# Kernel optimization log

Measured on AMD Instinct MI355X. Metric: run time of the kernel, lower is better.

The kernel has to match this reference:

```python
import jax, jax.numpy as jnp
import numpy as np

GAE_GAMMA = 0.99
GAE_LAMBDA = 0.95
T, N_ENVS = 4096, 2048


def setup_inputs() -> dict:
    key = jax.random.key(0)
    k1, k2, k3, k4 = jax.random.split(key, 4)
    rewards = jax.random.normal(k1, (T, N_ENVS), dtype=jnp.float32)
    values = jax.random.normal(k2, (T, N_ENVS), dtype=jnp.float32)
    next_values = jax.random.normal(k3, (T, N_ENVS), dtype=jnp.float32)
    next_dones = jax.random.randint(k4, (T, N_ENVS), 0, 2).astype(jnp.bool_)
    return {"rewards": rewards, "values": values,
            "next_values": next_values, "next_dones": next_dones}


def reference(rewards, values, next_values, next_dones):
    gamma = jnp.asarray(GAE_GAMMA, rewards.dtype)
    lam = jnp.asarray(GAE_LAMBDA, rewards.dtype)
    not_done = 1.0 - next_dones.astype(rewards.dtype)  # ~next_dones
    # deltas[t] = r[t] + gamma * V(s_{t+1}) * ~done[t] - V(s_t)
    deltas = rewards + gamma * next_values * not_done - values
    gae_discount = gamma * lam

    def step(running_gae, inp):
        delta_t, nd_t = inp
        g = delta_t + gae_discount * nd_t * running_gae
        return g, g

    init = jnp.zeros_like(rewards[0])
    # reverse-time scan over the recurrence
    _, adv = jax.lax.scan(step, init, (deltas, not_done), reverse=True)
    returns = adv + values
    return adv, returns
```

## Files before the change

kernel.cpp:

```cpp
#include <hip/hip_runtime.h>

#define TT    4096
#define NENV  2048
#define N4    (NENV / 4)
#define L     8
#define NCH   (TT / L)
#define TPCH  (NENV / 4)
#define NCGRP (TPCH / 256)
#define NBLK  (NCH * NCGRP)

#define GAMMA 0.99f
#define GL    (0.99f * 0.95f)

#define STEP_AB(r_, v_, nv_, dn_, A_, B_)                    \
    {                                                        \
        const float nd = (dn_) ? 0.0f : 1.0f;                \
        const float di = (r_) + GAMMA * (nv_) * nd - (v_);   \
        const float c  = GL * nd;                            \
        (B_) = di + c * (B_);                                \
        (A_) = c * (A_);                                     \
    }

#define STEP_OUT(r_, v_, nv_, dn_, g_, adv_, ret_)           \
    {                                                        \
        const float nd = (dn_) ? 0.0f : 1.0f;                \
        const float di = (r_) + GAMMA * (nv_) * nd - (v_);   \
        (g_) = di + GL * nd * (g_);                          \
        (adv_) = (g_);                                       \
        (ret_) = (g_) + (v_);                                \
    }

__global__ __launch_bounds__(256) void gae_k1(
    const float4* __restrict__ r4,
    const float4* __restrict__ v4,
    const float4* __restrict__ nv4,
    const int4*   __restrict__ dn4,
    float4* __restrict__ wsA,
    float4* __restrict__ wsB)
{
    const int chunk = blockIdx.x / NCGRP;
    const int c4    = (blockIdx.x % NCGRP) * 256 + threadIdx.x;
    const int t0    = chunk * L;

    float Ax = 1.0f, Ay = 1.0f, Az = 1.0f, Aw = 1.0f;
    float Bx = 0.0f, By = 0.0f, Bz = 0.0f, Bw = 0.0f;

#pragma unroll
    for (int i = L - 1; i >= 0; --i) {
        const int idx = (t0 + i) * N4 + c4;
        const float4 r  = r4[idx];
        const float4 v  = v4[idx];
        const float4 nv = nv4[idx];
        const int4   dn = dn4[idx];
        STEP_AB(r.x, v.x, nv.x, dn.x, Ax, Bx);
        STEP_AB(r.y, v.y, nv.y, dn.y, Ay, By);
        STEP_AB(r.z, v.z, nv.z, dn.z, Az, Bz);
        STEP_AB(r.w, v.w, nv.w, dn.w, Aw, Bw);
    }
    wsA[chunk * N4 + c4] = make_float4(Ax, Ay, Az, Aw);
    wsB[chunk * N4 + c4] = make_float4(Bx, By, Bz, Bw);
}

__global__ __launch_bounds__(256) void gae_k2(
    const float* __restrict__ wsA,
    const float* __restrict__ wsB,
    float* __restrict__ gIn)
{
    const int col = blockIdx.x * 256 + threadIdx.x;
    float g = 0.0f;
#pragma unroll 8
    for (int j = NCH - 1; j >= 0; --j) {
        gIn[j * NENV + col] = g;
        g = wsB[j * NENV + col] + wsA[j * NENV + col] * g;
    }
}

__global__ __launch_bounds__(256) void gae_k3(
    const float4* __restrict__ r4,
    const float4* __restrict__ v4,
    const float4* __restrict__ nv4,
    const int4*   __restrict__ dn4,
    const float4* __restrict__ gIn4,
    float4* __restrict__ adv4,
    float4* __restrict__ ret4)
{
    const int chunk = blockIdx.x / NCGRP;
    const int c4    = (blockIdx.x % NCGRP) * 256 + threadIdx.x;
    const int t0    = chunk * L;

    const float4 g0 = gIn4[chunk * N4 + c4];
    float gx = g0.x, gy = g0.y, gz = g0.z, gw = g0.w;

#pragma unroll
    for (int i = L - 1; i >= 0; --i) {
        const int idx = (t0 + i) * N4 + c4;
        const float4 r  = r4[idx];
        const float4 v  = v4[idx];
        const float4 nv = nv4[idx];
        const int4   dn = dn4[idx];
        float4 a, t;
        STEP_OUT(r.x, v.x, nv.x, dn.x, gx, a.x, t.x);
        STEP_OUT(r.y, v.y, nv.y, dn.y, gy, a.y, t.y);
        STEP_OUT(r.z, v.z, nv.z, dn.z, gz, a.z, t.z);
        STEP_OUT(r.w, v.w, nv.w, dn.w, gw, a.w, t.w);
        adv4[idx] = a;
        ret4[idx] = t;
    }
}

extern "C" void kernel_launch(void* const* d_in, const int* in_sizes, int n_in,
                              void* d_out, int out_size, void* d_ws, size_t ws_size,
                              hipStream_t stream) {
    const float4* r4  = (const float4*)d_in[0];
    const float4* v4  = (const float4*)d_in[1];
    const float4* nv4 = (const float4*)d_in[2];
    const int4*   dn4 = (const int4*)d_in[3];

    float4* adv4 = (float4*)d_out;
    float4* ret4 = adv4 + (size_t)TT * N4;

    float4* wsA = (float4*)d_ws;
    float4* wsB = wsA + (size_t)NCH * N4;
    float*  gIn = (float*)(wsB + (size_t)NCH * N4);

    gae_k1<<<NBLK, 256, 0, stream>>>(r4, v4, nv4, dn4, wsA, wsB);
    gae_k2<<<NENV / 256, 256, 0, stream>>>((const float*)wsA, (const float*)wsB, gIn);
    gae_k3<<<NBLK, 256, 0, stream>>>(r4, v4, nv4, dn4, (const float4*)gIn,
                                     adv4, ret4);
}
```

Baseline: 225.1 us.

## Fuse three GAE scan phases into one cooperative kernel with grid syncs

Merges the chunk-summary, cross-chunk carry and output phases into a single cooperative kernel separated by two grid-wide barriers. It uses 1024 resident blocks with a launch bound of 4 blocks per CU. The goal is to remove the launch gaps and tail drains between the three back-to-back kernels. The trade-off is the cost of the grid barriers and a host-side occupancy query on every launch. The middle phase still runs on only 8 blocks while the rest wait at the barrier, and the original three-kernel path is kept as a fallback.

```diff
diff --git a/kernel.cpp b/kernel.cpp
--- a/kernel.cpp
+++ b/kernel.cpp
@@ -1,12 +1,14 @@
 #include <hip/hip_runtime.h>
+#include <hip/hip_cooperative_groups.h>
+
+namespace cg = cooperative_groups;
 
 #define TT    4096
 #define NENV  2048
 #define N4    (NENV / 4)
 #define L     8
 #define NCH   (TT / L)
-#define TPCH  (NENV / 4)
-#define NCGRP (TPCH / 256)
+#define NCGRP 2
 #define NBLK  (NCH * NCGRP)
 
 #define GAMMA 0.99f
@@ -30,21 +32,87 @@
         (ret_) = (g_) + (v_);                                \
     }
 
-__global__ __launch_bounds__(256) void gae_k1(
+__global__ __launch_bounds__(256, 4) void gae_coop(
     const float4* __restrict__ r4,
     const float4* __restrict__ v4,
     const float4* __restrict__ nv4,
     const int4*   __restrict__ dn4,
+    float4* __restrict__ adv4,
+    float4* __restrict__ ret4,
     float4* __restrict__ wsA,
-    float4* __restrict__ wsB)
+    float4* __restrict__ wsB,
+    float*  __restrict__ gIn)
 {
     const int chunk = blockIdx.x / NCGRP;
     const int c4    = (blockIdx.x % NCGRP) * 256 + threadIdx.x;
     const int t0    = chunk * L;
 
+    {
+        float Ax = 1.0f, Ay = 1.0f, Az = 1.0f, Aw = 1.0f;
+        float Bx = 0.0f, By = 0.0f, Bz = 0.0f, Bw = 0.0f;
+#pragma unroll
+        for (int i = L - 1; i >= 0; --i) {
+            const int idx = (t0 + i) * N4 + c4;
+            const float4 r  = r4[idx];
+            const float4 v  = v4[idx];
+            const float4 nv = nv4[idx];
+            const int4   dn = dn4[idx];
+            STEP_AB(r.x, v.x, nv.x, dn.x, Ax, Bx);
+            STEP_AB(r.y, v.y, nv.y, dn.y, Ay, By);
+            STEP_AB(r.z, v.z, nv.z, dn.z, Az, Bz);
+            STEP_AB(r.w, v.w, nv.w, dn.w, Aw, Bw);
+        }
+        wsA[chunk * N4 + c4] = make_float4(Ax, Ay, Az, Aw);
+        wsB[chunk * N4 + c4] = make_float4(Bx, By, Bz, Bw);
+    }
+
+    cg::this_grid().sync();
+
+    if (blockIdx.x < NENV / 256) {
+        const int col = blockIdx.x * 256 + threadIdx.x;
+        const float* a = (const float*)wsA;
+        const float* b = (const float*)wsB;
+        float g = 0.0f;
+#pragma unroll 8
+        for (int j = NCH - 1; j >= 0; --j) {
+            gIn[j * NENV + col] = g;
+            g = b[j * NENV + col] + a[j * NENV + col] * g;
+        }
+    }
+
+    cg::this_grid().sync();
+
+    {
+        const float4 g0 = ((const float4*)gIn)[chunk * N4 + c4];
+        float gx = g0.x, gy = g0.y, gz = g0.z, gw = g0.w;
+#pragma unroll
+        for (int i = L - 1; i >= 0; --i) {
+            const int idx = (t0 + i) * N4 + c4;
+            const float4 r  = r4[idx];
+            const float4 v  = v4[idx];
+            const float4 nv = nv4[idx];
+            const int4   dn = dn4[idx];
+            float4 a, t;
+            STEP_OUT(r.x, v.x, nv.x, dn.x, gx, a.x, t.x);
+            STEP_OUT(r.y, v.y, nv.y, dn.y, gy, a.y, t.y);
+            STEP_OUT(r.z, v.z, nv.z, dn.z, gz, a.z, t.z);
+            STEP_OUT(r.w, v.w, nv.w, dn.w, gw, a.w, t.w);
+            adv4[idx] = a;
+            ret4[idx] = t;
+        }
+    }
+}
+
+__global__ __launch_bounds__(256) void gae_k1(
+    const float4* __restrict__ r4, const float4* __restrict__ v4,
+    const float4* __restrict__ nv4, const int4* __restrict__ dn4,
+    float4* __restrict__ wsA, float4* __restrict__ wsB)
+{
+    const int chunk = blockIdx.x / NCGRP;
+    const int c4    = (blockIdx.x % NCGRP) * 256 + threadIdx.x;
+    const int t0    = chunk * L;
     float Ax = 1.0f, Ay = 1.0f, Az = 1.0f, Aw = 1.0f;
     float Bx = 0.0f, By = 0.0f, Bz = 0.0f, Bw = 0.0f;
-
 #pragma unroll
     for (int i = L - 1; i >= 0; --i) {
         const int idx = (t0 + i) * N4 + c4;
@@ -62,8 +130,7 @@
 }
 
 __global__ __launch_bounds__(256) void gae_k2(
-    const float* __restrict__ wsA,
-    const float* __restrict__ wsB,
+    const float* __restrict__ wsA, const float* __restrict__ wsB,
     float* __restrict__ gIn)
 {
     const int col = blockIdx.x * 256 + threadIdx.x;
@@ -76,21 +143,16 @@
 }
 
 __global__ __launch_bounds__(256) void gae_k3(
-    const float4* __restrict__ r4,
-    const float4* __restrict__ v4,
-    const float4* __restrict__ nv4,
-    const int4*   __restrict__ dn4,
-    const float4* __restrict__ gIn4,
-    float4* __restrict__ adv4,
+    const float4* __restrict__ r4, const float4* __restrict__ v4,
+    const float4* __restrict__ nv4, const int4* __restrict__ dn4,
+    const float4* __restrict__ gIn4, float4* __restrict__ adv4,
     float4* __restrict__ ret4)
 {
     const int chunk = blockIdx.x / NCGRP;
     const int c4    = (blockIdx.x % NCGRP) * 256 + threadIdx.x;
     const int t0    = chunk * L;
-
     const float4 g0 = gIn4[chunk * N4 + c4];
     float gx = g0.x, gy = g0.y, gz = g0.z, gw = g0.w;
-
 #pragma unroll
     for (int i = L - 1; i >= 0; --i) {
         const int idx = (t0 + i) * N4 + c4;
@@ -123,8 +185,27 @@
     float4* wsB = wsA + (size_t)NCH * N4;
     float*  gIn = (float*)(wsB + (size_t)NCH * N4);
 
-    gae_k1<<<NBLK, 256, 0, stream>>>(r4, v4, nv4, dn4, wsA, wsB);
-    gae_k2<<<NENV / 256, 256, 0, stream>>>((const float*)wsA, (const float*)wsB, gIn);
-    gae_k3<<<NBLK, 256, 0, stream>>>(r4, v4, nv4, dn4, (const float4*)gIn,
-                                     adv4, ret4);
-}
+    int blocksPerCU = 0;
+    (void)hipOccupancyMaxActiveBlocksPerMultiprocessor(
+        &blocksPerCU, (const void*)gae_coop, 256, 0);
+    const bool coop_ok = (blocksPerCU * 256 >= NBLK);
+
+    bool launched = false;
+    if (coop_ok) {
+        void* args[] = {
+            (void*)&r4, (void*)&v4, (void*)&nv4, (void*)&dn4,
+            (void*)&adv4, (void*)&ret4, (void*)&wsA, (void*)&wsB, (void*)&gIn
+        };
+        hipError_t e = hipLaunchCooperativeKernel((const void*)gae_coop,
+                                                  dim3(NBLK), dim3(256),
+                                                  args, 0, stream);
+        launched = (e == hipSuccess);
+    }
+    if (!launched) {
+        gae_k1<<<NBLK, 256, 0, stream>>>(r4, v4, nv4, dn4, wsA, wsB);
+        gae_k2<<<NENV / 256, 256, 0, stream>>>((const float*)wsA,
+                                               (const float*)wsB, gIn);
+        gae_k3<<<NBLK, 256, 0, stream>>>(r4, v4, nv4, dn4, (const float4*)gIn,
+                                         adv4, ret4);
+    }
+}
```

Measured after the change: 225.2 us. About the same (+0.0%).

## Split serial chunk-carry scan into hierarchical super-chunk scan

Applied to the files above, without the earlier changes.

The single serial carry scan over all 512 chunks is replaced by three stages. First, a parallel kernel composes affine (A,B) carries within groups of 8 chunks. Next, a short serial scan runs over 64 super-chunks using more, smaller blocks. Finally, the output kernel recomposes the remaining intra-group carries before its local recurrence. This shortens the latency-bound dependent chain, at the cost of an extra launch and extra workspace reads in the final kernel.

```diff
diff --git a/kernel.cpp b/kernel.cpp
--- a/kernel.cpp
+++ b/kernel.cpp
@@ -5,9 +5,10 @@
 #define N4    (NENV / 4)
 #define L     8
 #define NCH   (TT / L)
-#define TPCH  (NENV / 4)
-#define NCGRP (TPCH / 256)
+#define NCGRP 2
 #define NBLK  (NCH * NCGRP)
+#define SUP   8
+#define NSUP  (NCH / SUP)
 
 #define GAMMA 0.99f
 #define GL    (0.99f * 0.95f)
@@ -30,13 +31,16 @@
         (ret_) = (g_) + (v_);                                \
     }
 
+#define COMPOSE(Aj_, Bj_, A_, B_)                            \
+    {                                                        \
+        (B_) = (Bj_) + (Aj_) * (B_);                         \
+        (A_) = (Aj_) * (A_);                                 \
+    }
+
 __global__ __launch_bounds__(256) void gae_k1(
-    const float4* __restrict__ r4,
-    const float4* __restrict__ v4,
-    const float4* __restrict__ nv4,
-    const int4*   __restrict__ dn4,
-    float4* __restrict__ wsA,
-    float4* __restrict__ wsB)
+    const float4* __restrict__ r4,  const float4* __restrict__ v4,
+    const float4* __restrict__ nv4, const int4*   __restrict__ dn4,
+    float4* __restrict__ wsA, float4* __restrict__ wsB)
 {
     const int chunk = blockIdx.x / NCGRP;
     const int c4    = (blockIdx.x % NCGRP) * 256 + threadIdx.x;
@@ -44,7 +48,6 @@
 
     float Ax = 1.0f, Ay = 1.0f, Az = 1.0f, Aw = 1.0f;
     float Bx = 0.0f, By = 0.0f, Bz = 0.0f, Bw = 0.0f;
-
 #pragma unroll
     for (int i = L - 1; i >= 0; --i) {
         const int idx = (t0 + i) * N4 + c4;
@@ -61,35 +64,64 @@
     wsB[chunk * N4 + c4] = make_float4(Bx, By, Bz, Bw);
 }
 
-__global__ __launch_bounds__(256) void gae_k2(
-    const float* __restrict__ wsA,
-    const float* __restrict__ wsB,
-    float* __restrict__ gIn)
+__global__ __launch_bounds__(256) void gae_k2a(
+    const float4* __restrict__ wsA, const float4* __restrict__ wsB,
+    float4* __restrict__ supA, float4* __restrict__ supB)
 {
-    const int col = blockIdx.x * 256 + threadIdx.x;
+    const int t  = blockIdx.x * 256 + threadIdx.x;
+    const int s  = t >> 9;
+    const int c4 = t & (N4 - 1);
+
+    float Ax = 1.0f, Ay = 1.0f, Az = 1.0f, Aw = 1.0f;
+    float Bx = 0.0f, By = 0.0f, Bz = 0.0f, Bw = 0.0f;
+#pragma unroll
+    for (int j = s * SUP + SUP - 1; j >= s * SUP; --j) {
+        const float4 Aj = wsA[j * N4 + c4];
+        const float4 Bj = wsB[j * N4 + c4];
+        COMPOSE(Aj.x, Bj.x, Ax, Bx);
+        COMPOSE(Aj.y, Bj.y, Ay, By);
+        COMPOSE(Aj.z, Bj.z, Az, Bz);
+        COMPOSE(Aj.w, Bj.w, Aw, Bw);
+    }
+    supA[s * N4 + c4] = make_float4(Ax, Ay, Az, Aw);
+    supB[s * N4 + c4] = make_float4(Bx, By, Bz, Bw);
+}
+
+__global__ __launch_bounds__(64) void gae_k2b(
+    const float* __restrict__ supA, const float* __restrict__ supB,
+    float* __restrict__ gSup)
+{
+    const int col = blockIdx.x * 64 + threadIdx.x;
     float g = 0.0f;
 #pragma unroll 8
-    for (int j = NCH - 1; j >= 0; --j) {
-        gIn[j * NENV + col] = g;
-        g = wsB[j * NENV + col] + wsA[j * NENV + col] * g;
+    for (int s = NSUP - 1; s >= 0; --s) {
+        gSup[s * NENV + col] = g;
+        g = supB[s * NENV + col] + supA[s * NENV + col] * g;
     }
 }
 
 __global__ __launch_bounds__(256) void gae_k3(
-    const float4* __restrict__ r4,
-    const float4* __restrict__ v4,
-    const float4* __restrict__ nv4,
-    const int4*   __restrict__ dn4,
-    const float4* __restrict__ gIn4,
-    float4* __restrict__ adv4,
-    float4* __restrict__ ret4)
+    const float4* __restrict__ r4,  const float4* __restrict__ v4,
+    const float4* __restrict__ nv4, const int4*   __restrict__ dn4,
+    const float4* __restrict__ wsA, const float4* __restrict__ wsB,
+    const float4* __restrict__ gSup4,
+    float4* __restrict__ adv4, float4* __restrict__ ret4)
 {
     const int chunk = blockIdx.x / NCGRP;
     const int c4    = (blockIdx.x % NCGRP) * 256 + threadIdx.x;
+    const int s     = chunk / SUP;
     const int t0    = chunk * L;
 
-    const float4 g0 = gIn4[chunk * N4 + c4];
+    const float4 g0 = gSup4[s * N4 + c4];
     float gx = g0.x, gy = g0.y, gz = g0.z, gw = g0.w;
+    for (int j = s * SUP + SUP - 1; j > chunk; --j) {
+        const float4 Aj = wsA[j * N4 + c4];
+        const float4 Bj = wsB[j * N4 + c4];
+        gx = Bj.x + Aj.x * gx;
+        gy = Bj.y + Aj.y * gy;
+        gz = Bj.z + Aj.z * gz;
+        gw = Bj.w + Aj.w * gw;
+    }
 
 #pragma unroll
     for (int i = L - 1; i >= 0; --i) {
@@ -119,12 +151,16 @@
     float4* adv4 = (float4*)d_out;
     float4* ret4 = adv4 + (size_t)TT * N4;
 
-    float4* wsA = (float4*)d_ws;
-    float4* wsB = wsA + (size_t)NCH * N4;
-    float*  gIn = (float*)(wsB + (size_t)NCH * N4);
+    float4* wsA  = (float4*)d_ws;
+    float4* wsB  = wsA  + (size_t)NCH * N4;
+    float4* supA = wsB  + (size_t)NCH * N4;
+    float4* supB = supA + (size_t)NSUP * N4;
+    float4* gSup = supB + (size_t)NSUP * N4;
 
     gae_k1<<<NBLK, 256, 0, stream>>>(r4, v4, nv4, dn4, wsA, wsB);
-    gae_k2<<<NENV / 256, 256, 0, stream>>>((const float*)wsA, (const float*)wsB, gIn);
-    gae_k3<<<NBLK, 256, 0, stream>>>(r4, v4, nv4, dn4, (const float4*)gIn,
-                                     adv4, ret4);
+    gae_k2a<<<(NSUP * N4) / 256, 256, 0, stream>>>(wsA, wsB, supA, supB);
+    gae_k2b<<<NENV / 64, 64, 0, stream>>>((const float*)supA, (const float*)supB,
+                                          (float*)gSup);
+    gae_k3<<<NBLK, 256, 0, stream>>>(r4, v4, nv4, dn4, wsA, wsB,
+                                     (const float4*)gSup, adv4, ret4);
 }
```

Result: faster. 204.2 us (-9.3%).
